# Optimization experiments

Hardware: AMD Instinct MI355X
Metric: run time of the kernel (lower is better)

## Reference

```python
import jax, jax.numpy as jnp
import numpy as np

N_NODES = 100000
N_EDGES = 1000000
IN_CH = 128
OUT_CH = 128
T_DIM = 64


def setup_inputs() -> dict:
    key = jax.random.key(0)
    ks = jax.random.split(key, 9)
    x = jax.random.normal(ks[0], (N_NODES, IN_CH), dtype=jnp.float32)
    edge_index = jax.random.randint(ks[1], (2, N_EDGES), 0, N_NODES, dtype=jnp.int64)
    temporal_features = jax.random.normal(ks[2], (N_EDGES, T_DIM), dtype=jnp.float32)
    # Learned params (torch nn.Linear convention: weight [out, in], bias [out])
    s = 1.0 / np.sqrt(IN_CH)
    st = 1.0 / np.sqrt(T_DIM)
    W_S_w = jax.random.uniform(ks[3], (OUT_CH, IN_CH), minval=-s, maxval=s, dtype=jnp.float32)
    W_S_b = jax.random.uniform(ks[4], (OUT_CH,), minval=-s, maxval=s, dtype=jnp.float32)
    W_T_w = jax.random.uniform(ks[5], (OUT_CH, IN_CH), minval=-s, maxval=s, dtype=jnp.float32)
    W_T_b = jax.random.uniform(ks[6], (OUT_CH,), minval=-s, maxval=s, dtype=jnp.float32)
    T_w = jax.random.uniform(ks[7], (OUT_CH, T_DIM), minval=-st, maxval=st, dtype=jnp.float32)
    T_b = jax.random.uniform(ks[8], (OUT_CH,), minval=-st, maxval=st, dtype=jnp.float32)
    return {
        "x": x, "edge_index": edge_index, "temporal_features": temporal_features,
        "W_S_w": W_S_w, "W_S_b": W_S_b, "W_T_w": W_T_w, "W_T_b": W_T_b,
        "T_w": T_w, "T_b": T_b,
    }


def reference(x, edge_index, temporal_features, W_S_w, W_S_b, W_T_w, W_T_b, T_w, T_b):
    num_nodes = x.shape[0]
    row, col = edge_index[0], edge_index[1]
    # self transform: [N, out]
    self_features = x @ W_S_w.T + W_S_b
    # gather neighbor feats then transform: [E, out]
    neighbor_features = x[col] @ W_T_w.T + W_T_b
    # temporal encodings: [E, out]
    temporal_encodings = temporal_features @ T_w.T + T_b
    messages = neighbor_features + temporal_encodings
    # scatter-add aggregation over destination nodes
    aggregated = jax.ops.segment_sum(messages, row, num_segments=num_nodes)
    return jax.nn.relu(self_features + aggregated)
```

## Files before the change

kernel.cpp:

```cpp
#include <hip/hip_runtime.h>

#define N_NODES 100000
#define M_PAD   100096
#define N_EDGES 1000000
#define K_TOT   320
#define NCHUNK  98

#define BM  128

#define XCONV_THREADS 1600000
#define PREP_BLOCKS   6410
#define HIST_BLOCKS   3907

typedef __attribute__((ext_vector_type(8))) short bf16x8;
typedef __attribute__((ext_vector_type(4))) float f32x4;

__device__ __forceinline__ unsigned short f2bf(float f) {
    unsigned u = __float_as_uint(f);
    u += 0x7FFFu + ((u >> 16) & 1u);
    return (unsigned short)(u >> 16);
}
__device__ __forceinline__ unsigned pack2(float a, float b) {
    return (unsigned)f2bf(a) | ((unsigned)f2bf(b) << 16);
}
__device__ __forceinline__ float bflo(unsigned v) { return __uint_as_float(v << 16); }
__device__ __forceinline__ float bfhi(unsigned v) { return __uint_as_float(v & 0xffff0000u); }

__device__ __forceinline__ void gl_lds16(const void* g, void* l) {
    __builtin_amdgcn_global_load_lds(
        (const __attribute__((address_space(1))) unsigned*)g,
        (__attribute__((address_space(3))) unsigned*)l, 16, 0, 0);
}

__global__ __launch_bounds__(256) void prep_hist_kernel(
        const float* __restrict__ x,
        const float* __restrict__ WSw,
        const float* __restrict__ WTw,
        const float* __restrict__ Tw,
        const float* __restrict__ WTb,
        const float* __restrict__ Tb,
        unsigned short* __restrict__ xb,
        unsigned short* __restrict__ Gtb,
        float* __restrict__ bias2,
        const int* __restrict__ ei,
        int* __restrict__ hist) {
    int b = blockIdx.x;
    int t = threadIdx.x;
    if (b >= PREP_BLOCKS) {
        int e = (b - PREP_BLOCKS) * 256 + t;
        if (e < N_EDGES) atomicAdd(&hist[ei[e]], 1);
        return;
    }
    int gid = b * 256 + t;
    if (gid < XCONV_THREADS) {
        const float4* p = (const float4*)x + (size_t)gid * 2;
        float4 u0 = p[0], u1 = p[1];
        uint4 w;
        w.x = pack2(u0.x, u0.y);
        w.y = pack2(u0.z, u0.w);
        w.z = pack2(u1.x, u1.y);
        w.w = pack2(u1.z, u1.w);
        *(uint4*)(xb + (size_t)gid * 8) = w;
    } else {
        int idx = gid - XCONV_THREADS;
        if (idx < K_TOT * 128) {
            int k = idx >> 7;
            int o = idx & 127;
            float v = (k < 128) ? WSw[o * 128 + k]
                    : (k < 256) ? WTw[o * 128 + (k - 128)]
                                : Tw[o * 64 + (k - 256)];
            Gtb[(size_t)o * K_TOT + k] = f2bf(v);
        }
        if (idx < 128) bias2[idx] = WTb[idx] + Tb[idx];
    }
}

__global__ __launch_bounds__(256) void scan_pass1(const int* __restrict__ hist,
                                                  int* __restrict__ chunksum) {
    __shared__ int ts[256];
    int b = blockIdx.x, t = threadIdx.x;
    int i = b * 1024 + t * 4;
    int s = 0;
#pragma unroll
    for (int j = 0; j < 4; ++j)
        if (i + j < N_NODES) s += hist[i + j];
    ts[t] = s;
    __syncthreads();
    for (int off = 128; off > 0; off >>= 1) {
        if (t < off) ts[t] += ts[t + off];
        __syncthreads();
    }
    if (t == 0) chunksum[b] = ts[0];
}

__global__ __launch_bounds__(256) void scan_pass2(const int* __restrict__ hist,
                                                  const int* __restrict__ csum,
                                                  int* __restrict__ offsets) {
    __shared__ int ts[256];
    __shared__ int cbase_s;
    int b = blockIdx.x, t = threadIdx.x;
    int i0 = b * 1024 + t * 4;
    int v[4];
    int s = 0;
#pragma unroll
    for (int j = 0; j < 4; ++j) {
        v[j] = (i0 + j < N_NODES) ? hist[i0 + j] : 0;
        s += v[j];
    }
    ts[t] = s;
    if (t < 64) {
        int cs = 0;
        for (int i = t; i < b; i += 64) cs += csum[i];
        for (int off = 32; off; off >>= 1) cs += __shfl_down(cs, off);
        if (t == 0) cbase_s = cs;
    }
    __syncthreads();
    for (int off = 1; off < 256; off <<= 1) {
        int add = (t >= off) ? ts[t - off] : 0;
        __syncthreads();
        ts[t] += add;
        __syncthreads();
    }
    int run = cbase_s + ts[t] - s;
#pragma unroll
    for (int j = 0; j < 4; ++j) {
        if (i0 + j < N_NODES) offsets[i0 + j] = run;
        run += v[j];
    }
}

__global__ __launch_bounds__(256) void fill_kernel(const int* __restrict__ ei,
                                                   int* __restrict__ offsets,
                                                   unsigned long long* __restrict__ ec) {
    int e = blockIdx.x * 256 + threadIdx.x;
    if (e < N_EDGES) {
        int row = ei[e];
        int col = ei[N_EDGES + e];
        int pos = atomicAdd(&offsets[row], 1);
        ec[pos] = ((unsigned long long)(unsigned)col << 32) | (unsigned)e;
    }
}

__global__ __launch_bounds__(256) void agg_kernel(
        const unsigned* __restrict__ xw,
        const float* __restrict__ tf,
        const unsigned long long* __restrict__ ec,
        const int* __restrict__ offsets,
        unsigned* __restrict__ aggxb,
        unsigned* __restrict__ aggtb,
        float* __restrict__ deg) {
    int lane = threadIdx.x & 63;
    int n = blockIdx.x * 4 + (threadIdx.x >> 6);

    int beg = n ? offsets[n - 1] : 0;
    int end = offsets[n];

    float ax[4] = {0.f, 0.f, 0.f, 0.f};
    float ay[4] = {0.f, 0.f, 0.f, 0.f};
    float at[4] = {0.f, 0.f, 0.f, 0.f};

    int i = beg;
    for (; i + 7 < end; i += 8) {
        unsigned long long p[8];
#pragma unroll
        for (int j = 0; j < 8; ++j) p[j] = ec[i + j];
        unsigned xv[8];
        float tv[8];
#pragma unroll
        for (int j = 0; j < 8; ++j)
            xv[j] = xw[((size_t)(p[j] >> 32) << 6) + lane];
#pragma unroll
        for (int j = 0; j < 8; ++j)
            tv[j] = __builtin_nontemporal_load(tf + ((size_t)(unsigned)p[j] << 6) + lane);
#pragma unroll
        for (int j = 0; j < 8; ++j) {
            ax[j & 3] += bflo(xv[j]);
            ay[j & 3] += bfhi(xv[j]);
            at[j & 3] += tv[j];
        }
    }
    int rem = end - i;
    if (rem) {
        int last = end - 1;
        unsigned long long p[8];
#pragma unroll
        for (int j = 0; j < 8; ++j) {
            int idx = i + j;
            if (idx > last) idx = last;
            p[j] = ec[idx];
        }
        unsigned xv[8];
        float tv[8];
#pragma unroll
        for (int j = 0; j < 8; ++j)
            xv[j] = xw[((size_t)(p[j] >> 32) << 6) + lane];
#pragma unroll
        for (int j = 0; j < 8; ++j)
            tv[j] = __builtin_nontemporal_load(tf + ((size_t)(unsigned)p[j] << 6) + lane);
#pragma unroll
        for (int j = 0; j < 8; ++j) {
            if (j < rem) {
                ax[j & 3] += bflo(xv[j]);
                ay[j & 3] += bfhi(xv[j]);
                at[j & 3] += tv[j];
            }
        }
    }

    float fx = (ax[0] + ax[1]) + (ax[2] + ax[3]);
    float fy = (ay[0] + ay[1]) + (ay[2] + ay[3]);
    float ft = (at[0] + at[1]) + (at[2] + at[3]);
    aggxb[(size_t)n * 64 + lane] = pack2(fx, fy);
    float pt = __shfl_xor(ft, 1);
    if (!(lane & 1))
        aggtb[(size_t)n * 32 + (lane >> 1)] = pack2(ft, pt);
    if (lane == 0) deg[n] = (float)(end - beg);
}

__global__ __launch_bounds__(256) void gemm_kernel(
        const unsigned short* __restrict__ xb,
        const unsigned short* __restrict__ aggxb,
        const unsigned short* __restrict__ aggtb,
        const unsigned short* __restrict__ Gtb,
        const float* __restrict__ WSb,
        const float* __restrict__ bias2,
        const float* __restrict__ deg,
        float* __restrict__ out) {
    __shared__ unsigned short As[BM * 64];
    __shared__ unsigned short Bs[BM * 64];

    int t = threadIdx.x;
    int lane = t & 63;
    int wave = t >> 6;
    int mw = (wave & 1) * 64;
    int nw = (wave >> 1) * 64;
    int row0 = blockIdx.x * BM;
    int quad = lane >> 4;
    int l16  = lane & 15;

    int lr = lane >> 3;
    int lc = lane & 7;
    int swz = ((lc ^ lr) << 4);

    f32x4 acc[4][4];
#pragma unroll
    for (int mt = 0; mt < 4; ++mt)
#pragma unroll
        for (int nt = 0; nt < 4; ++nt)
            acc[mt][nt] = (f32x4){0.f, 0.f, 0.f, 0.f};

    for (int c = 0; c < 5; ++c) {
        const char* srcA; size_t ldb, koffb;
        if (c < 2)      { srcA = (const char*)xb;    ldb = 256; koffb = (size_t)c * 128; }
        else if (c < 4) { srcA = (const char*)aggxb; ldb = 256; koffb = (size_t)(c - 2) * 128; }
        else            { srcA = (const char*)aggtb; ldb = 128; koffb = 0; }

        __syncthreads();
#pragma unroll
        for (int j = 0; j < 4; ++j) {
            int r = wave * 4 + j;
            int row = r * 8 + lr;
            gl_lds16(srcA + (size_t)(row0 + row) * ldb + koffb + swz,
                     (char*)As + r * 1024);
            gl_lds16((const char*)Gtb + (size_t)row * 640 + (size_t)c * 128 + swz,
                     (char*)Bs + r * 1024);
        }
        __syncthreads();

#pragma unroll
        for (int ks = 0; ks < 2; ++ks) {
            bf16x8 af[4], bfv[4];
            int rb = ((ks * 64 + quad * 16) ^ ((l16 & 7) << 4));
#pragma unroll
            for (int mt = 0; mt < 4; ++mt)
                af[mt] = *(const bf16x8*)((const char*)As + (mw + mt * 16 + l16) * 128 + rb);
#pragma unroll
            for (int nt = 0; nt < 4; ++nt)
                bfv[nt] = *(const bf16x8*)((const char*)Bs + (nw + nt * 16 + l16) * 128 + rb);
#pragma unroll
            for (int mt = 0; mt < 4; ++mt)
#pragma unroll
                for (int nt = 0; nt < 4; ++nt)
                    acc[mt][nt] = __builtin_amdgcn_mfma_f32_16x16x32_bf16(
                        af[mt], bfv[nt], acc[mt][nt], 0, 0, 0);
        }
    }

    float wsb[4], b2[4];
#pragma unroll
    for (int nt = 0; nt < 4; ++nt) {
        int o = nw + nt * 16 + l16;
        wsb[nt] = WSb[o];
        b2[nt]  = bias2[o];
    }
#pragma unroll
    for (int mt = 0; mt < 4; ++mt) {
#pragma unroll
        for (int r = 0; r < 4; ++r) {
            int m = row0 + mw + mt * 16 + quad * 4 + r;
            if (m >= N_NODES) continue;
            float dg = deg[m];
#pragma unroll
            for (int nt = 0; nt < 4; ++nt) {
                int o = nw + nt * 16 + l16;
                float val = acc[mt][nt][r] + wsb[nt] + dg * b2[nt];
                __builtin_nontemporal_store(fmaxf(val, 0.f), &out[(size_t)m * 128 + o]);
            }
        }
    }
}

extern "C" void kernel_launch(void* const* d_in, const int* in_sizes, int n_in,
                              void* d_out, int out_size, void* d_ws, size_t ws_size,
                              hipStream_t stream) {
    const float* x   = (const float*)d_in[0];
    const int*   ei  = (const int*)d_in[1];
    const float* tf  = (const float*)d_in[2];
    const float* WSw = (const float*)d_in[3];
    const float* WSb = (const float*)d_in[4];
    const float* WTw = (const float*)d_in[5];
    const float* WTb = (const float*)d_in[6];
    const float* Tw  = (const float*)d_in[7];
    const float* Tb  = (const float*)d_in[8];
    float* out = (float*)d_out;

    unsigned short* xb    = (unsigned short*)d_ws;
    unsigned short* aggxb = xb    + (size_t)M_PAD * 128;
    unsigned short* aggtb = aggxb + (size_t)M_PAD * 128;
    unsigned short* Gtb   = aggtb + (size_t)M_PAD * 64;
    unsigned long long* ec = (unsigned long long*)(Gtb + (size_t)K_TOT * 128);
    float* deg   = (float*)(ec + N_EDGES);
    float* bias2 = deg + N_NODES;
    int* hist    = (int*)(bias2 + 128);
    int* offsets = hist + N_NODES;
    int* csum    = offsets + (N_NODES + 2);

    hipMemsetAsync(hist, 0, (size_t)N_NODES * sizeof(int), stream);

    prep_hist_kernel<<<PREP_BLOCKS + HIST_BLOCKS, 256, 0, stream>>>(
        x, WSw, WTw, Tw, WTb, Tb, xb, Gtb, bias2, ei, hist);

    scan_pass1<<<NCHUNK, 256, 0, stream>>>(hist, csum);
    scan_pass2<<<NCHUNK, 256, 0, stream>>>(hist, csum, offsets);

    fill_kernel<<<(N_EDGES + 255) / 256, 256, 0, stream>>>(ei, offsets, ec);

    agg_kernel<<<N_NODES / 4, 256, 0, stream>>>(
        (const unsigned*)xb, tf, ec, offsets, (unsigned*)aggxb, (unsigned*)aggtb, deg);

    gemm_kernel<<<(N_NODES + BM - 1) / BM, 256, 0, stream>>>(
        xb, aggxb, aggtb, Gtb, WSb, bias2, deg, out);
}
```

Before: 575.4 us.

## Fuse neighbor aggregation into GEMM kernel via LDS-resident aggregates

Merges the aggregation and GEMM kernels into one. Each 512-thread block gathers the neighbor and temporal sums for its 128 nodes directly into swizzled LDS, then runs the MFMA GEMM with 8 waves. The aggregated features and degree array no longer make a round trip through global memory, and one launch is removed. In exchange the block count drops to about 782 large blocks with heavy LDS use, each wave walks 16 nodes serially, and the GEMM cannot overlap the gather phase within a block, so occupancy and latency hiding may suffer.

```diff
diff --git a/kernel.cpp b/kernel.cpp
--- a/kernel.cpp
+++ b/kernel.cpp
@@ -141,154 +141,172 @@
     }
 }
 
-__global__ __launch_bounds__(256) void agg_kernel(
-        const unsigned* __restrict__ xw,
+__global__ __launch_bounds__(512, 4) void agg_gemm_kernel(
         const float* __restrict__ tf,
         const unsigned long long* __restrict__ ec,
         const int* __restrict__ offsets,
-        unsigned* __restrict__ aggxb,
-        unsigned* __restrict__ aggtb,
-        float* __restrict__ deg) {
-    int lane = threadIdx.x & 63;
-    int n = blockIdx.x * 4 + (threadIdx.x >> 6);
-
-    int beg = n ? offsets[n - 1] : 0;
-    int end = offsets[n];
-
-    float ax[4] = {0.f, 0.f, 0.f, 0.f};
-    float ay[4] = {0.f, 0.f, 0.f, 0.f};
-    float at[4] = {0.f, 0.f, 0.f, 0.f};
-
-    int i = beg;
-    for (; i + 7 < end; i += 8) {
-        unsigned long long p[8];
-#pragma unroll
-        for (int j = 0; j < 8; ++j) p[j] = ec[i + j];
-        unsigned xv[8];
-        float tv[8];
-#pragma unroll
-        for (int j = 0; j < 8; ++j)
-            xv[j] = xw[((size_t)(p[j] >> 32) << 6) + lane];
-#pragma unroll
-        for (int j = 0; j < 8; ++j)
-            tv[j] = __builtin_nontemporal_load(tf + ((size_t)(unsigned)p[j] << 6) + lane);
-#pragma unroll
-        for (int j = 0; j < 8; ++j) {
-            ax[j & 3] += bflo(xv[j]);
-            ay[j & 3] += bfhi(xv[j]);
-            at[j & 3] += tv[j];
-        }
-    }
-    int rem = end - i;
-    if (rem) {
-        int last = end - 1;
-        unsigned long long p[8];
-#pragma unroll
-        for (int j = 0; j < 8; ++j) {
-            int idx = i + j;
-            if (idx > last) idx = last;
-            p[j] = ec[idx];
-        }
-        unsigned xv[8];
-        float tv[8];
-#pragma unroll
-        for (int j = 0; j < 8; ++j)
-            xv[j] = xw[((size_t)(p[j] >> 32) << 6) + lane];
-#pragma unroll
-        for (int j = 0; j < 8; ++j)
-            tv[j] = __builtin_nontemporal_load(tf + ((size_t)(unsigned)p[j] << 6) + lane);
-#pragma unroll
-        for (int j = 0; j < 8; ++j) {
-            if (j < rem) {
+        const unsigned short* __restrict__ xb,
+        const unsigned short* __restrict__ Gtb,
+        const float* __restrict__ WSb,
+        const float* __restrict__ bias2,
+        float* __restrict__ out) {
+    __shared__ unsigned short As[BM * 64];
+    __shared__ unsigned short Bs[BM * 64];
+    __shared__ unsigned aggx_lds[BM * 64];
+    __shared__ unsigned aggt_lds[BM * 32];
+
+    const unsigned* xw = (const unsigned*)xb;
+
+    int t = threadIdx.x;
+    int lane = t & 63;
+    int wave = t >> 6;
+    int row0 = blockIdx.x * BM;
+
+    int lr = lane >> 3;
+    int lc = lane & 7;
+    int swz = ((lc ^ lr) << 4);
+
+#pragma unroll
+    for (int j = 0; j < 2; ++j) {
+        int r = wave * 2 + j;
+        int row = r * 8 + lr;
+        gl_lds16((const char*)xb + (size_t)(row0 + row) * 256 + swz,
+                 (char*)As + r * 1024);
+        gl_lds16((const char*)Gtb + (size_t)row * 640 + swz,
+                 (char*)Bs + r * 1024);
+    }
+
+    for (int q = 0; q < 16; ++q) {
+        int m = wave * 16 + q;
+        int n = row0 + m;
+        int beg = 0, end = 0;
+        if (n < N_NODES) {
+            beg = n ? offsets[n - 1] : 0;
+            end = offsets[n];
+        }
+
+        float ax[4] = {0.f, 0.f, 0.f, 0.f};
+        float ay[4] = {0.f, 0.f, 0.f, 0.f};
+        float at[4] = {0.f, 0.f, 0.f, 0.f};
+
+        int i = beg;
+        for (; i + 7 < end; i += 8) {
+            unsigned long long p[8];
+#pragma unroll
+            for (int j = 0; j < 8; ++j) p[j] = ec[i + j];
+            unsigned xv[8];
+            float tv[8];
+#pragma unroll
+            for (int j = 0; j < 8; ++j)
+                xv[j] = xw[((size_t)(p[j] >> 32) << 6) + lane];
+#pragma unroll
+            for (int j = 0; j < 8; ++j)
+                tv[j] = __builtin_nontemporal_load(tf + ((size_t)(unsigned)p[j] << 6) + lane);
+#pragma unroll
+            for (int j = 0; j < 8; ++j) {
                 ax[j & 3] += bflo(xv[j]);
                 ay[j & 3] += bfhi(xv[j]);
                 at[j & 3] += tv[j];
             }
         }
-    }
-
-    float fx = (ax[0] + ax[1]) + (ax[2] + ax[3]);
-    float fy = (ay[0] + ay[1]) + (ay[2] + ay[3]);
-    float ft = (at[0] + at[1]) + (at[2] + at[3]);
-    aggxb[(size_t)n * 64 + lane] = pack2(fx, fy);
-    float pt = __shfl_xor(ft, 1);
-    if (!(lane & 1))
-        aggtb[(size_t)n * 32 + (lane >> 1)] = pack2(ft, pt);
-    if (lane == 0) deg[n] = (float)(end - beg);
-}
-
-__global__ __launch_bounds__(256) void gemm_kernel(
-        const unsigned short* __restrict__ xb,
-        const unsigned short* __restrict__ aggxb,
-        const unsigned short* __restrict__ aggtb,
-        const unsigned short* __restrict__ Gtb,
-        const float* __restrict__ WSb,
-        const float* __restrict__ bias2,
-        const float* __restrict__ deg,
-        float* __restrict__ out) {
-    __shared__ unsigned short As[BM * 64];
-    __shared__ unsigned short Bs[BM * 64];
-
-    int t = threadIdx.x;
-    int lane = t & 63;
-    int wave = t >> 6;
-    int mw = (wave & 1) * 64;
-    int nw = (wave >> 1) * 64;
-    int row0 = blockIdx.x * BM;
+        int rem = end - i;
+        if (rem) {
+            int last = end - 1;
+            unsigned long long p[8];
+#pragma unroll
+            for (int j = 0; j < 8; ++j) {
+                int idx = i + j;
+                if (idx > last) idx = last;
+                p[j] = ec[idx];
+            }
+            unsigned xv[8];
+            float tv[8];
+#pragma unroll
+            for (int j = 0; j < 8; ++j)
+                xv[j] = xw[((size_t)(p[j] >> 32) << 6) + lane];
+#pragma unroll
+            for (int j = 0; j < 8; ++j)
+                tv[j] = __builtin_nontemporal_load(tf + ((size_t)(unsigned)p[j] << 6) + lane);
+#pragma unroll
+            for (int j = 0; j < 8; ++j) {
+                if (j < rem) {
+                    ax[j & 3] += bflo(xv[j]);
+                    ay[j & 3] += bfhi(xv[j]);
+                    at[j & 3] += tv[j];
+                }
+            }
+        }
+
+        float fx = (ax[0] + ax[1]) + (ax[2] + ax[3]);
+        float fy = (ay[0] + ay[1]) + (ay[2] + ay[3]);
+        float ft = (at[0] + at[1]) + (at[2] + at[3]);
+
+        aggx_lds[m * 64 + (lane >> 5) * 32 + ((lane & 31) ^ ((m & 7) << 2))] =
+            pack2(fx, fy);
+        float pt = __shfl_xor(ft, 1);
+        if (!(lane & 1))
+            aggt_lds[m * 32 + ((lane >> 1) ^ ((m & 7) << 2))] = pack2(ft, pt);
+    }
+
+    __syncthreads();
+
     int quad = lane >> 4;
     int l16  = lane & 15;
-
-    int lr = lane >> 3;
-    int lc = lane & 7;
-    int swz = ((lc ^ lr) << 4);
-
-    f32x4 acc[4][4];
+    int mw = (wave >> 2) * 64;
+    int nw = (wave & 3) * 32;
+
+    f32x4 acc[4][2];
 #pragma unroll
     for (int mt = 0; mt < 4; ++mt)
 #pragma unroll
-        for (int nt = 0; nt < 4; ++nt)
+        for (int nt = 0; nt < 2; ++nt)
             acc[mt][nt] = (f32x4){0.f, 0.f, 0.f, 0.f};
 
     for (int c = 0; c < 5; ++c) {
-        const char* srcA; size_t ldb, koffb;
-        if (c < 2)      { srcA = (const char*)xb;    ldb = 256; koffb = (size_t)c * 128; }
-        else if (c < 4) { srcA = (const char*)aggxb; ldb = 256; koffb = (size_t)(c - 2) * 128; }
-        else            { srcA = (const char*)aggtb; ldb = 128; koffb = 0; }
-
-        __syncthreads();
-#pragma unroll
-        for (int j = 0; j < 4; ++j) {
-            int r = wave * 4 + j;
-            int row = r * 8 + lr;
-            gl_lds16(srcA + (size_t)(row0 + row) * ldb + koffb + swz,
-                     (char*)As + r * 1024);
-            gl_lds16((const char*)Gtb + (size_t)row * 640 + (size_t)c * 128 + swz,
-                     (char*)Bs + r * 1024);
-        }
-        __syncthreads();
-
 #pragma unroll
         for (int ks = 0; ks < 2; ++ks) {
-            bf16x8 af[4], bfv[4];
             int rb = ((ks * 64 + quad * 16) ^ ((l16 & 7) << 4));
+            bf16x8 af[4], bfv[2];
+#pragma unroll
+            for (int mt = 0; mt < 4; ++mt) {
+                int row = mw + mt * 16 + l16;
+                const char* ap;
+                if (c < 2)      ap = (const char*)As + row * 128 + rb;
+                else if (c < 4) ap = (const char*)aggx_lds + row * 256 + (c - 2) * 128 + rb;
+                else            ap = (const char*)aggt_lds + row * 128 + rb;
+                af[mt] = *(const bf16x8*)ap;
+            }
+#pragma unroll
+            for (int nt = 0; nt < 2; ++nt)
+                bfv[nt] = *(const bf16x8*)((const char*)Bs + (nw + nt * 16 + l16) * 128 + rb);
 #pragma unroll
             for (int mt = 0; mt < 4; ++mt)
-                af[mt] = *(const bf16x8*)((const char*)As + (mw + mt * 16 + l16) * 128 + rb);
-#pragma unroll
-            for (int nt = 0; nt < 4; ++nt)
-                bfv[nt] = *(const bf16x8*)((const char*)Bs + (nw + nt * 16 + l16) * 128 + rb);
-#pragma unroll
-            for (int mt = 0; mt < 4; ++mt)
-#pragma unroll
-                for (int nt = 0; nt < 4; ++nt)
+#pragma unroll
+                for (int nt = 0; nt < 2; ++nt)
                     acc[mt][nt] = __builtin_amdgcn_mfma_f32_16x16x32_bf16(
                         af[mt], bfv[nt], acc[mt][nt], 0, 0, 0);
         }
-    }
-
-    float wsb[4], b2[4];
-#pragma unroll
-    for (int nt = 0; nt < 4; ++nt) {
+        if (c < 4) {
+            __syncthreads();
+#pragma unroll
+            for (int j = 0; j < 2; ++j) {
+                int r = wave * 2 + j;
+                int row = r * 8 + lr;
+                if (c + 1 < 2)
+                    gl_lds16((const char*)xb + (size_t)(row0 + row) * 256 +
+                                 (size_t)(c + 1) * 128 + swz,
+                             (char*)As + r * 1024);
+                gl_lds16((const char*)Gtb + (size_t)row * 640 +
+                             (size_t)(c + 1) * 128 + swz,
+                         (char*)Bs + r * 1024);
+            }
+            __syncthreads();
+        }
+    }
+
+    float wsb[2], b2[2];
+#pragma unroll
+    for (int nt = 0; nt < 2; ++nt) {
         int o = nw + nt * 16 + l16;
         wsb[nt] = WSb[o];
         b2[nt]  = bias2[o];
@@ -299,9 +317,9 @@
         for (int r = 0; r < 4; ++r) {
             int m = row0 + mw + mt * 16 + quad * 4 + r;
             if (m >= N_NODES) continue;
-            float dg = deg[m];
-#pragma unroll
-            for (int nt = 0; nt < 4; ++nt) {
+            float dg = (float)(offsets[m] - (m ? offsets[m - 1] : 0));
+#pragma unroll
+            for (int nt = 0; nt < 2; ++nt) {
                 int o = nw + nt * 16 + l16;
                 float val = acc[mt][nt][r] + wsb[nt] + dg * b2[nt];
                 __builtin_nontemporal_store(fmaxf(val, 0.f), &out[(size_t)m * 128 + o]);
@@ -324,13 +342,10 @@
     const float* Tb  = (const float*)d_in[8];
     float* out = (float*)d_out;
 
-    unsigned short* xb    = (unsigned short*)d_ws;
-    unsigned short* aggxb = xb    + (size_t)M_PAD * 128;
-    unsigned short* aggtb = aggxb + (size_t)M_PAD * 128;
-    unsigned short* Gtb   = aggtb + (size_t)M_PAD * 64;
+    unsigned short* xb  = (unsigned short*)d_ws;
+    unsigned short* Gtb = xb + (size_t)M_PAD * 128;
     unsigned long long* ec = (unsigned long long*)(Gtb + (size_t)K_TOT * 128);
-    float* deg   = (float*)(ec + N_EDGES);
-    float* bias2 = deg + N_NODES;
+    float* bias2 = (float*)(ec + N_EDGES);
     int* hist    = (int*)(bias2 + 128);
     int* offsets = hist + N_NODES;
     int* csum    = offsets + (N_NODES + 2);
@@ -345,9 +360,6 @@
 
     fill_kernel<<<(N_EDGES + 255) / 256, 256, 0, stream>>>(ei, offsets, ec);
 
-    agg_kernel<<<N_NODES / 4, 256, 0, stream>>>(
-        (const unsigned*)xb, tf, ec, offsets, (unsigned*)aggxb, (unsigned*)aggtb, deg);
-
-    gemm_kernel<<<(N_NODES + BM - 1) / BM, 256, 0, stream>>>(
-        xb, aggxb, aggtb, Gtb, WSb, bias2, deg, out);
-}
+    agg_gemm_kernel<<<M_PAD / BM, 512, 0, stream>>>(
+        tf, ec, offsets, xb, Gtb, WSb, bias2, out);
+}
```

Result: slower. 611.6 us (+6.3%).
